# Optimization experiments

Hardware: AMD Instinct MI355X
Metric: run time of the kernel (lower is better)

Reference implementation:

```python
import jax, jax.numpy as jnp
import numpy as np

B, T_EN, T_DE, D_EN, D_DE, UNITS = 16, 256, 256, 512, 512, 128


def setup_inputs() -> dict:
    key = jax.random.key(0)
    k1, k2, k3, k4, k5 = jax.random.split(key, 5)
    # glorot-uniform style scale for weights
    def glorot(k, shape):
        lim = np.sqrt(6.0 / (shape[0] + shape[1]))
        return jax.random.uniform(k, shape, jnp.float32, -lim, lim)
    return {
        "en_seq": jax.random.normal(k1, (B, T_EN, D_EN), jnp.float32),
        "de_seq": jax.random.normal(k2, (B, T_DE, D_DE), jnp.float32),
        "w_en": glorot(k3, (D_EN, UNITS)),
        "w_de": glorot(k4, (D_DE, UNITS)),
        "nu": glorot(k5, (UNITS, 1)),
    }


def reference(en_seq, de_seq, w_en, w_de, nu):
    # Additive (Bahdanau) time attention.
    # Original keras code builds the (de, en) cross product via K.repeat /
    # K.repeat_elements with de-major, en-minor ordering; equivalent to
    # broadcasting att_de over a new en axis and att_en over a new de axis.
    att_en = jnp.einsum("bie,eu->biu", en_seq, w_en)   # (B, T_en, U)
    att_de = jnp.einsum("bjd,du->bju", de_seq, w_de)   # (B, T_de, U)
    # co_m: (B, T_de, T_en, U) — the large broadcast intermediate
    co_m = jnp.tanh(att_de[:, :, None, :] + att_en[:, None, :, :])
    mu = jnp.einsum("bjiu,u->bji", co_m, nu[:, 0])      # (B, T_de, T_en)
    alphas = jax.nn.softmax(mu, axis=-1)                # softmax over encoder time
    sum_en = jnp.einsum("bji,bie->bje", alphas, en_seq)  # (B, T_de, D_en)
    return jnp.concatenate([de_seq, sum_en], axis=-1)    # (B, T_de, D_de + D_en)
```

## Files before the change

kernel.cpp:

```cpp
#include <hip/hip_runtime.h>
#include <hip/hip_bf16.h>

#define TANH_SCALE 2.8853900817779268f


__device__ __forceinline__ void gemm_tile_32x128(
        const float* __restrict__ X, const float* __restrict__ W,
        int row0, int k0, int k1, int tid, float acc[4][4],
        float (*xt)[36], float (*wsh)[128]) {
    const int xs_r  = tid >> 4;
    const int xs_k4 = (tid & 15) * 4;
    float4 xr[2], wr[8];

    auto g_load = [&](int kt) {
#pragma unroll
        for (int s = 0; s < 2; ++s)
            xr[s] = *reinterpret_cast<const float4*>(
                X + (size_t)(row0 + xs_r + 16 * s) * 512 + kt + xs_k4);
#pragma unroll
        for (int s = 0; s < 8; ++s) {
            int idx = tid + 256 * s;
            wr[s] = *reinterpret_cast<const float4*>(
                W + (size_t)(kt + (idx >> 5)) * 128 + (idx & 31) * 4);
        }
    };
    auto lds_store = [&]() {
        const int swz = ((xs_k4 >> 2) & 7) << 2;
#pragma unroll
        for (int s = 0; s < 2; ++s) {
            int r = (xs_r + 16 * s) ^ swz;
            xt[xs_k4 + 0][r] = xr[s].x;
            xt[xs_k4 + 1][r] = xr[s].y;
            xt[xs_k4 + 2][r] = xr[s].z;
            xt[xs_k4 + 3][r] = xr[s].w;
        }
#pragma unroll
        for (int s = 0; s < 8; ++s) {
            int idx = tid + 256 * s;
            *reinterpret_cast<float4*>(&wsh[idx >> 5][(idx & 31) * 4]) = wr[s];
        }
    };

    const int tr = tid >> 5, tc = tid & 31;
    g_load(k0);
    lds_store();
    __syncthreads();
    for (int kt = k0; kt < k1; kt += 64) {
        const bool has_next = (kt + 64) < k1;
        if (has_next) g_load(kt + 64);
#pragma unroll
        for (int k = 0; k < 64; ++k) {
            const int col = (tr * 4) ^ (((k >> 2) & 7) << 2);
            float4 xv = *reinterpret_cast<const float4*>(&xt[k][col]);
            float4 wv = *reinterpret_cast<const float4*>(&wsh[k][tc * 4]);
            acc[0][0] = fmaf(xv.x, wv.x, acc[0][0]);
            acc[0][1] = fmaf(xv.x, wv.y, acc[0][1]);
            acc[0][2] = fmaf(xv.x, wv.z, acc[0][2]);
            acc[0][3] = fmaf(xv.x, wv.w, acc[0][3]);
            acc[1][0] = fmaf(xv.y, wv.x, acc[1][0]);
            acc[1][1] = fmaf(xv.y, wv.y, acc[1][1]);
            acc[1][2] = fmaf(xv.y, wv.z, acc[1][2]);
            acc[1][3] = fmaf(xv.y, wv.w, acc[1][3]);
            acc[2][0] = fmaf(xv.z, wv.x, acc[2][0]);
            acc[2][1] = fmaf(xv.z, wv.y, acc[2][1]);
            acc[2][2] = fmaf(xv.z, wv.z, acc[2][2]);
            acc[2][3] = fmaf(xv.z, wv.w, acc[2][3]);
            acc[3][0] = fmaf(xv.w, wv.x, acc[3][0]);
            acc[3][1] = fmaf(xv.w, wv.y, acc[3][1]);
            acc[3][2] = fmaf(xv.w, wv.z, acc[3][2]);
            acc[3][3] = fmaf(xv.w, wv.w, acc[3][3]);
        }
        __syncthreads();
        if (has_next) {
            lds_store();
            __syncthreads();
        }
    }
}

__global__ __launch_bounds__(256) void proj_split_kernel(
        const float* __restrict__ en, const float* __restrict__ de,
        const float* __restrict__ w_en, const float* __restrict__ w_de,
        float* __restrict__ P) {
    __shared__ float xt[64][36];
    __shared__ float wsh[64][128];
    const bool is_en = (blockIdx.y == 0);
    const float* X = is_en ? en : de;
    const float* W = is_en ? w_en : w_de;
    const int row0 = blockIdx.x * 32;
    const int kq   = blockIdx.z;

    float acc[4][4] = {{0.f}};
    gemm_tile_32x128(X, W, row0, kq * 256, kq * 256 + 256, threadIdx.x,
                     acc, xt, wsh);

    float* OUT = P + (size_t)(blockIdx.y * 2 + kq) * 524288;
    const int tr = threadIdx.x >> 5, tc = threadIdx.x & 31;
#pragma unroll
    for (int r = 0; r < 4; ++r)
        *reinterpret_cast<float4*>(OUT + (size_t)(row0 + tr * 4 + r) * 128 + tc * 4)
            = make_float4(acc[r][0], acc[r][1], acc[r][2], acc[r][3]);
}

__global__ __launch_bounds__(256) void combine_kernel(
        const float* __restrict__ P, float* __restrict__ Ete,
        float* __restrict__ Ede) {
    const int gid = blockIdx.x * 256 + threadIdx.x;
    const float* Pm = P + (size_t)blockIdx.y * 1048576;
    float4 a = reinterpret_cast<const float4*>(Pm)[gid];
    float4 b = reinterpret_cast<const float4*>(Pm + 524288)[gid];
    float4 v;
    v.x = __builtin_exp2f(-TANH_SCALE * (a.x + b.x));
    v.y = __builtin_exp2f(-TANH_SCALE * (a.y + b.y));
    v.z = __builtin_exp2f(-TANH_SCALE * (a.z + b.z));
    v.w = __builtin_exp2f(-TANH_SCALE * (a.w + b.w));
    if (blockIdx.y == 1) {
        reinterpret_cast<float4*>(Ede)[gid] = v;
    } else {
        const int row = gid >> 5, u4 = gid & 31;
        const int b_ = row >> 8, i = row & 255;
        float* base = Ete + (size_t)b_ * 32768 + (size_t)(u4 * 2) * 512 + i * 2;
        *reinterpret_cast<float2*>(base)       = make_float2(v.x, v.y);
        *reinterpret_cast<float2*>(base + 512) = make_float2(v.z, v.w);
    }
}

__global__ __launch_bounds__(256) void proj_full_kernel(
        const float* __restrict__ en, const float* __restrict__ de,
        const float* __restrict__ w_en, const float* __restrict__ w_de,
        float* __restrict__ Ete, float* __restrict__ Ede) {
    __shared__ float xt[64][36];
    __shared__ float wsh[64][128];
    const bool is_en = (blockIdx.y == 0);
    const float* X = is_en ? en : de;
    const float* W = is_en ? w_en : w_de;
    const int row0 = blockIdx.x * 32;

    float acc[4][4] = {{0.f}};
    gemm_tile_32x128(X, W, row0, 0, 512, threadIdx.x, acc, xt, wsh);

    const int tr = threadIdx.x >> 5, tc = threadIdx.x & 31;
    float v[4][4];
#pragma unroll
    for (int r = 0; r < 4; ++r)
#pragma unroll
        for (int c = 0; c < 4; ++c)
            v[r][c] = __builtin_exp2f(-TANH_SCALE * acc[r][c]);

    if (!is_en) {
#pragma unroll
        for (int r = 0; r < 4; ++r)
            *reinterpret_cast<float4*>(
                Ede + (size_t)(row0 + tr * 4 + r) * 128 + tc * 4) =
                make_float4(v[r][0], v[r][1], v[r][2], v[r][3]);
    } else {
        const int b_ = row0 >> 8;
        const int il0 = (row0 & 255) + tr * 4;
#pragma unroll
        for (int cp = 0; cp < 2; ++cp) {
            size_t base = (size_t)b_ * 32768 + (size_t)(tc * 2 + cp) * 512 + il0 * 2;
            *reinterpret_cast<float4*>(Ete + base) =
                make_float4(v[0][2 * cp], v[0][2 * cp + 1],
                            v[1][2 * cp], v[1][2 * cp + 1]);
            *reinterpret_cast<float4*>(Ete + base + 4) =
                make_float4(v[2][2 * cp], v[2][2 * cp + 1],
                            v[3][2 * cp], v[3][2 * cp + 1]);
        }
    }
}

__global__ __launch_bounds__(512, 4) void fused_attn_kernel(
        const float* __restrict__ Ete, const float* __restrict__ Ede,
        const float* __restrict__ nu, const float* __restrict__ en,
        const float* __restrict__ de, float* __restrict__ out) {
    const int phys = blockIdx.x;
    const int lid  = (phys & 7) * 64 + (phys >> 3);
    const int b    = lid >> 5;
    const int j0   = (lid & 31) * 8;
    const int tid  = threadIdx.x;
    const int i    = tid & 255;
    const int uh   = tid >> 8;

    __shared__ float ede_sh[8][128];
    __shared__ float nu2_sh[128];
    __shared__ float nusum_sh[64];
    __shared__ float al[8][256];
    __shared__ float red[8][4];

    if (tid < 256)
        reinterpret_cast<float4*>(&ede_sh[0][0])[tid] =
            reinterpret_cast<const float4*>(Ede + ((size_t)b * 256 + j0) * 128)[tid];
    if (tid >= 256 && tid < 384) nu2_sh[tid - 256] = 2.0f * nu[tid - 256];
    if (tid >= 384 && tid < 448) {
        int t = tid - 384;
        nusum_sh[t] = 2.0f * (nu[2 * t] + nu[2 * t + 1]);
    }

    {
        const float4* dsrc =
            reinterpret_cast<const float4*>(de + ((size_t)b * 256 + j0) * 512);
#pragma unroll
        for (int t = 0; t < 2; ++t) {
            int idx = tid + 512 * t;
            int j = idx >> 7, c4 = idx & 127;
            reinterpret_cast<float4*>(out + (size_t)(b * 256 + j0 + j) * 1024)[c4] =
                dsrc[idx];
        }
    }
    __syncthreads();

    float s[4] = {0.0f, 0.0f, 0.0f, 0.0f};
    const float2* ep =
        reinterpret_cast<const float2*>(Ete) + (size_t)b * 16384 + i;
    const float4* nu4 = reinterpret_cast<const float4*>(nu2_sh);
    const float4* cs4 = reinterpret_cast<const float4*>(nusum_sh);

    float2 evc[4], evn[4];
#pragma unroll
    for (int t = 0; t < 4; ++t) evc[t] = ep[t * 256];
    for (int q = 0; q < 16; ++q) {
        if (q < 15) {
#pragma unroll
            for (int t = 0; t < 4; ++t) evn[t] = ep[(4 * (q + 1) + t) * 256];
        }
        const float4 na = nu4[2 * q];
        const float4 nb = nu4[2 * q + 1];
        const float4 cs = cs4[q];
#pragma unroll
        for (int jl = 0; jl < 4; ++jl) {
            const float* dr = &ede_sh[uh * 4 + jl][8 * q];
            const float4 da = *reinterpret_cast<const float4*>(dr);
            const float4 db = *reinterpret_cast<const float4*>(dr + 4);
            float e0, e1, den, num;
            e0 = evc[0].x * da.x; e1 = evc[0].y * da.y;
            den = 1.0f + e0; den = fmaf(den, e1, den);
            num = fmaf(na.x, e1, cs.x); num = fmaf(na.y, e0, num);
            s[jl] = fmaf(num, __builtin_amdgcn_rcpf(den), s[jl]);
            e0 = evc[1].x * da.z; e1 = evc[1].y * da.w;
            den = 1.0f + e0; den = fmaf(den, e1, den);
            num = fmaf(na.z, e1, cs.y); num = fmaf(na.w, e0, num);
            s[jl] = fmaf(num, __builtin_amdgcn_rcpf(den), s[jl]);
            e0 = evc[2].x * db.x; e1 = evc[2].y * db.y;
            den = 1.0f + e0; den = fmaf(den, e1, den);
            num = fmaf(nb.x, e1, cs.z); num = fmaf(nb.y, e0, num);
            s[jl] = fmaf(num, __builtin_amdgcn_rcpf(den), s[jl]);
            e0 = evc[3].x * db.z; e1 = evc[3].y * db.w;
            den = 1.0f + e0; den = fmaf(den, e1, den);
            num = fmaf(nb.z, e1, cs.w); num = fmaf(nb.w, e0, num);
            s[jl] = fmaf(num, __builtin_amdgcn_rcpf(den), s[jl]);
        }
        if (q < 15) {
#pragma unroll
            for (int t = 0; t < 4; ++t) evc[t] = evn[t];
        }
    }

    float p[4];
#pragma unroll
    for (int jl = 0; jl < 4; ++jl) p[jl] = __expf(s[jl]);
    const int lane = tid & 63;
    const int w    = (tid >> 6) & 3;
#pragma unroll
    for (int jl = 0; jl < 4; ++jl) {
        float t = p[jl];
#pragma unroll
        for (int off = 32; off >= 1; off >>= 1) t += __shfl_xor(t, off);
        if (lane == 0) red[uh * 4 + jl][w] = t;
    }
    __syncthreads();
#pragma unroll
    for (int jl = 0; jl < 4; ++jl) {
        const int j = uh * 4 + jl;
        float T = red[j][0] + red[j][1] + red[j][2] + red[j][3];
        al[j][i] = p[jl] * __builtin_amdgcn_rcpf(T);
    }
    __syncthreads();

    float acc[8];
#pragma unroll
    for (int j = 0; j < 8; ++j) acc[j] = 0.0f;
    const float* enb = en + (size_t)b * 256 * 512;
    const int c = tid;
    for (int i0 = 0; i0 < 256; i0 += 4) {
        float a[8][4];
#pragma unroll
        for (int j = 0; j < 8; ++j) {
            float4 v = *reinterpret_cast<const float4*>(&al[j][i0]);
            a[j][0] = v.x; a[j][1] = v.y; a[j][2] = v.z; a[j][3] = v.w;
        }
#pragma unroll
        for (int ii = 0; ii < 4; ++ii) {
            float e0 = enb[(size_t)(i0 + ii) * 512 + c];
#pragma unroll
            for (int j = 0; j < 8; ++j)
                acc[j] = fmaf(a[j][ii], e0, acc[j]);
        }
    }
#pragma unroll
    for (int j = 0; j < 8; ++j) {
        size_t row = (size_t)(b * 256 + j0 + j);
        out[row * 1024 + 512 + c] = acc[j];
    }
}

extern "C" void kernel_launch(void* const* d_in, const int* in_sizes, int n_in,
                              void* d_out, int out_size, void* d_ws, size_t ws_size,
                              hipStream_t stream) {
    const float* en   = (const float*)d_in[0];
    const float* de   = (const float*)d_in[1];
    const float* w_en = (const float*)d_in[2];
    const float* w_de = (const float*)d_in[3];
    const float* nu   = (const float*)d_in[4];
    float* out = (float*)d_out;

    char* ws = (char*)d_ws;
    float* Ete = (float*)(ws);
    float* Ede = (float*)(ws + (size_t)2 * 1024 * 1024);
    float* P   = (float*)(ws + (size_t)4 * 1024 * 1024);

    const bool split = ws_size >= (size_t)12 * 1024 * 1024;
    if (split) {
        proj_split_kernel<<<dim3(128, 2, 2), 256, 0, stream>>>(
            en, de, w_en, w_de, P);
        combine_kernel<<<dim3(512, 2), 256, 0, stream>>>(P, Ete, Ede);
    } else {
        proj_full_kernel<<<dim3(128, 2), 256, 0, stream>>>(
            en, de, w_en, w_de, Ete, Ede);
    }
    fused_attn_kernel<<<dim3(512), 512, 0, stream>>>(Ete, Ede, nu, en, de, out);
}
```

Baseline: 162.1 us.

## Halve rows per attention block and allow four-way split-K projection

The fused attention kernel now handles 4 decoder rows per block instead of 8, which doubles the grid to 1024 blocks so more waves can run on the GPU. The projection GEMM can now split K four ways when the workspace is large enough, and the combine kernel sums a variable number of partials. The cost is that each block reloads the Ete slice and the encoder rows for half as much work, and the combine step reads more partial buffers.

```diff
diff --git a/kernel.cpp b/kernel.cpp
--- a/kernel.cpp
+++ b/kernel.cpp
@@ -88,13 +88,14 @@
     const float* X = is_en ? en : de;
     const float* W = is_en ? w_en : w_de;
     const int row0 = blockIdx.x * 32;
-    const int kq   = blockIdx.z;
+    const int ns   = gridDim.z;
+    const int klen = 512 / ns;
+    const int k0   = blockIdx.z * klen;
 
     float acc[4][4] = {{0.f}};
-    gemm_tile_32x128(X, W, row0, kq * 256, kq * 256 + 256, threadIdx.x,
-                     acc, xt, wsh);
-
-    float* OUT = P + (size_t)(blockIdx.y * 2 + kq) * 524288;
+    gemm_tile_32x128(X, W, row0, k0, k0 + klen, threadIdx.x, acc, xt, wsh);
+
+    float* OUT = P + (size_t)(blockIdx.y * ns + blockIdx.z) * 524288;
     const int tr = threadIdx.x >> 5, tc = threadIdx.x & 31;
 #pragma unroll
     for (int r = 0; r < 4; ++r)
@@ -104,16 +105,19 @@
 
 __global__ __launch_bounds__(256) void combine_kernel(
         const float* __restrict__ P, float* __restrict__ Ete,
-        float* __restrict__ Ede) {
+        float* __restrict__ Ede, int nsplit) {
     const int gid = blockIdx.x * 256 + threadIdx.x;
-    const float* Pm = P + (size_t)blockIdx.y * 1048576;
+    const float* Pm = P + (size_t)blockIdx.y * nsplit * 524288;
     float4 a = reinterpret_cast<const float4*>(Pm)[gid];
-    float4 b = reinterpret_cast<const float4*>(Pm + 524288)[gid];
+    for (int t = 1; t < nsplit; ++t) {
+        float4 x = reinterpret_cast<const float4*>(Pm + (size_t)t * 524288)[gid];
+        a.x += x.x; a.y += x.y; a.z += x.z; a.w += x.w;
+    }
     float4 v;
-    v.x = __builtin_exp2f(-TANH_SCALE * (a.x + b.x));
-    v.y = __builtin_exp2f(-TANH_SCALE * (a.y + b.y));
-    v.z = __builtin_exp2f(-TANH_SCALE * (a.z + b.z));
-    v.w = __builtin_exp2f(-TANH_SCALE * (a.w + b.w));
+    v.x = __builtin_exp2f(-TANH_SCALE * a.x);
+    v.y = __builtin_exp2f(-TANH_SCALE * a.y);
+    v.z = __builtin_exp2f(-TANH_SCALE * a.z);
+    v.w = __builtin_exp2f(-TANH_SCALE * a.w);
     if (blockIdx.y == 1) {
         reinterpret_cast<float4*>(Ede)[gid] = v;
     } else {
@@ -174,42 +178,38 @@
         const float* __restrict__ nu, const float* __restrict__ en,
         const float* __restrict__ de, float* __restrict__ out) {
     const int phys = blockIdx.x;
-    const int lid  = (phys & 7) * 64 + (phys >> 3);
-    const int b    = lid >> 5;
-    const int j0   = (lid & 31) * 8;
+    const int lid  = (phys & 7) * 128 + (phys >> 3);
+    const int b    = lid >> 6;
+    const int j0   = (lid & 63) * 4;
     const int tid  = threadIdx.x;
     const int i    = tid & 255;
     const int uh   = tid >> 8;
 
-    __shared__ float ede_sh[8][128];
+    __shared__ float ede_sh[4][128];
     __shared__ float nu2_sh[128];
     __shared__ float nusum_sh[64];
-    __shared__ float al[8][256];
-    __shared__ float red[8][4];
-
-    if (tid < 256)
+    __shared__ float al[4][256];
+    __shared__ float red[4][4];
+
+    if (tid < 128)
         reinterpret_cast<float4*>(&ede_sh[0][0])[tid] =
             reinterpret_cast<const float4*>(Ede + ((size_t)b * 256 + j0) * 128)[tid];
-    if (tid >= 256 && tid < 384) nu2_sh[tid - 256] = 2.0f * nu[tid - 256];
-    if (tid >= 384 && tid < 448) {
-        int t = tid - 384;
+    if (tid >= 128 && tid < 256) nu2_sh[tid - 128] = 2.0f * nu[tid - 128];
+    if (tid >= 256 && tid < 320) {
+        int t = tid - 256;
         nusum_sh[t] = 2.0f * (nu[2 * t] + nu[2 * t + 1]);
     }
 
     {
         const float4* dsrc =
             reinterpret_cast<const float4*>(de + ((size_t)b * 256 + j0) * 512);
-#pragma unroll
-        for (int t = 0; t < 2; ++t) {
-            int idx = tid + 512 * t;
-            int j = idx >> 7, c4 = idx & 127;
-            reinterpret_cast<float4*>(out + (size_t)(b * 256 + j0 + j) * 1024)[c4] =
-                dsrc[idx];
-        }
+        int j = tid >> 7, c4 = tid & 127;
+        reinterpret_cast<float4*>(out + (size_t)(b * 256 + j0 + j) * 1024)[c4] =
+            dsrc[tid];
     }
     __syncthreads();
 
-    float s[4] = {0.0f, 0.0f, 0.0f, 0.0f};
+    float s[2] = {0.0f, 0.0f};
     const float2* ep =
         reinterpret_cast<const float2*>(Ete) + (size_t)b * 16384 + i;
     const float4* nu4 = reinterpret_cast<const float4*>(nu2_sh);
@@ -227,8 +227,8 @@
         const float4 nb = nu4[2 * q + 1];
         const float4 cs = cs4[q];
 #pragma unroll
-        for (int jl = 0; jl < 4; ++jl) {
-            const float* dr = &ede_sh[uh * 4 + jl][8 * q];
+        for (int jl = 0; jl < 2; ++jl) {
+            const float* dr = &ede_sh[uh * 2 + jl][8 * q];
             const float4 da = *reinterpret_cast<const float4*>(dr);
             const float4 db = *reinterpret_cast<const float4*>(dr + 4);
             float e0, e1, den, num;
@@ -255,36 +255,36 @@
         }
     }
 
-    float p[4];
-#pragma unroll
-    for (int jl = 0; jl < 4; ++jl) p[jl] = __expf(s[jl]);
+    float p[2];
+#pragma unroll
+    for (int jl = 0; jl < 2; ++jl) p[jl] = __expf(s[jl]);
     const int lane = tid & 63;
     const int w    = (tid >> 6) & 3;
 #pragma unroll
-    for (int jl = 0; jl < 4; ++jl) {
+    for (int jl = 0; jl < 2; ++jl) {
         float t = p[jl];
 #pragma unroll
         for (int off = 32; off >= 1; off >>= 1) t += __shfl_xor(t, off);
-        if (lane == 0) red[uh * 4 + jl][w] = t;
+        if (lane == 0) red[uh * 2 + jl][w] = t;
     }
     __syncthreads();
 #pragma unroll
-    for (int jl = 0; jl < 4; ++jl) {
-        const int j = uh * 4 + jl;
+    for (int jl = 0; jl < 2; ++jl) {
+        const int j = uh * 2 + jl;
         float T = red[j][0] + red[j][1] + red[j][2] + red[j][3];
         al[j][i] = p[jl] * __builtin_amdgcn_rcpf(T);
     }
     __syncthreads();
 
-    float acc[8];
-#pragma unroll
-    for (int j = 0; j < 8; ++j) acc[j] = 0.0f;
+    float acc[4];
+#pragma unroll
+    for (int j = 0; j < 4; ++j) acc[j] = 0.0f;
     const float* enb = en + (size_t)b * 256 * 512;
     const int c = tid;
     for (int i0 = 0; i0 < 256; i0 += 4) {
-        float a[8][4];
-#pragma unroll
-        for (int j = 0; j < 8; ++j) {
+        float a[4][4];
+#pragma unroll
+        for (int j = 0; j < 4; ++j) {
             float4 v = *reinterpret_cast<const float4*>(&al[j][i0]);
             a[j][0] = v.x; a[j][1] = v.y; a[j][2] = v.z; a[j][3] = v.w;
         }
@@ -292,12 +292,12 @@
         for (int ii = 0; ii < 4; ++ii) {
             float e0 = enb[(size_t)(i0 + ii) * 512 + c];
 #pragma unroll
-            for (int j = 0; j < 8; ++j)
+            for (int j = 0; j < 4; ++j)
                 acc[j] = fmaf(a[j][ii], e0, acc[j]);
         }
     }
 #pragma unroll
-    for (int j = 0; j < 8; ++j) {
+    for (int j = 0; j < 4; ++j) {
         size_t row = (size_t)(b * 256 + j0 + j);
         out[row * 1024 + 512 + c] = acc[j];
     }
@@ -318,14 +318,17 @@
     float* Ede = (float*)(ws + (size_t)2 * 1024 * 1024);
     float* P   = (float*)(ws + (size_t)4 * 1024 * 1024);
 
-    const bool split = ws_size >= (size_t)12 * 1024 * 1024;
-    if (split) {
-        proj_split_kernel<<<dim3(128, 2, 2), 256, 0, stream>>>(
+    int nsplit = 0;
+    if (ws_size >= (size_t)20 * 1024 * 1024)      nsplit = 4;
+    else if (ws_size >= (size_t)12 * 1024 * 1024) nsplit = 2;
+
+    if (nsplit) {
+        proj_split_kernel<<<dim3(128, 2, nsplit), 256, 0, stream>>>(
             en, de, w_en, w_de, P);
-        combine_kernel<<<dim3(512, 2), 256, 0, stream>>>(P, Ete, Ede);
+        combine_kernel<<<dim3(512, 2), 256, 0, stream>>>(P, Ete, Ede, nsplit);
     } else {
         proj_full_kernel<<<dim3(128, 2), 256, 0, stream>>>(
             en, de, w_en, w_de, Ete, Ede);
     }
-    fused_attn_kernel<<<dim3(512), 512, 0, stream>>>(Ete, Ede, nu, en, de, out);
-}
+    fused_attn_kernel<<<dim3(1024), 512, 0, stream>>>(Ete, Ede, nu, en, de, out);
+}
```

Measured after the change: 163.3 us. About the same (+0.8%).
